# Kernel tuning notes

Measured on AMD Instinct MI355X. Metric: run time of the kernel, lower is better.

## Reference

```python
import jax, jax.numpy as jnp
import numpy as np

H = W = 32
K = 3


def _im2col(a):
    # a: [B, C, H, W] -> patches [B, H*W, C*K*K], channel-major (c, kh, kw)
    # matching torch.nn.Unfold ordering.
    a_pad = jnp.pad(a, ((0, 0), (0, 0), (1, 1), (1, 1)), mode='reflect')  # [B,C,H+2,W+2]
    cols = jnp.stack(
        [a_pad[:, :, kh:kh + H, kw:kw + W] for kh in range(K) for kw in range(K)],
        axis=2,
    )  # [B, C, 9, H, W]
    B, C = a.shape[0], a.shape[1]
    cols = cols.reshape(B, C * K * K, H * W)  # [B, 576, 1024]
    return jnp.swapaxes(cols, 1, 2)  # [B, 1024, 576]


def setup_inputs() -> dict:
    key = jax.random.key(0)
    k1, k2 = jax.random.split(key)
    a = jax.random.normal(k1, (256, 64, 32, 32), dtype=jnp.float32)
    # kaiming_uniform fan_in = 576 -> bound = sqrt(6/576)
    bound = float(np.sqrt(6.0 / 576.0))
    conv_kernel = jax.random.uniform(k2, (576, 64), dtype=jnp.float32,
                                     minval=-bound, maxval=bound)
    return {"a": a, "conv_kernel": conv_kernel}


def reference(a, conv_kernel):
    patches = _im2col(a)  # [B, 1024, 576]
    mean = jnp.mean(patches, axis=-1, keepdims=True)
    std = jnp.std(patches, axis=-1, keepdims=True, ddof=1)  # torch unbiased std
    normed = (patches - mean) / std
    out = jnp.einsum('blp,po->blo', normed, conv_kernel)  # [B, 1024, 64]
    # Fold with 1x1 kernel == reshape back to [B, 64, 32, 32]
    out = jnp.swapaxes(out, 1, 2).reshape(a.shape[0], conv_kernel.shape[1], H, W)
    return out
```

## Files before the change

kernel.cpp:

```cpp
#include <hip/hip_runtime.h>


#define STRIDE 68
#define NROW   10
#define NPIX   320

typedef __attribute__((ext_vector_type(8))) short bf16x8;
typedef __attribute__((ext_vector_type(4))) short bf16x4;
typedef __attribute__((ext_vector_type(4))) float f32x4;

__device__ __forceinline__ unsigned short f2bf(float f) {
    union { float f; unsigned u; } v; v.f = f;
    unsigned r = v.u + 0x7FFFu + ((v.u >> 16) & 1u);
    return (unsigned short)(r >> 16);
}

__device__ __forceinline__ int reflect32(int x) {
    x = (x < 0) ? -x : x;
    return (x > 31) ? (62 - x) : x;
}

__global__ void prep_kernel(const float* __restrict__ W, uint4* __restrict__ wf,
                            float* __restrict__ scolg) {
    if (blockIdx.x == 18) {
        __shared__ float red[256];
        int t = threadIdx.x;
        int o = t & 63, kq = t >> 6;
        float s = 0.f;
        for (int k = kq * 144; k < kq * 144 + 144; ++k) {
            union { unsigned u; float f; } cv;
            cv.u = ((unsigned)f2bf(W[k * 64 + o])) << 16;
            s += cv.f;
        }
        red[t] = s;
        __syncthreads();
        if (t < 64) scolg[t] = red[t] + red[t + 64] + red[t + 128] + red[t + 192];
        return;
    }
    int idx = blockIdx.x * 256 + threadIdx.x;
    int lane = idx & 63;
    int ks   = (idx >> 6) % 18;
    int ntg  = idx / 1152;
    int quad = lane >> 4;
    int o    = ntg * 16 + (lane & 15);
    unsigned short v[8];
    #pragma unroll
    for (int j = 0; j < 8; ++j) {
        int kp = ks * 32 + quad * 8 + j;
        int c  = kp & 63;
        int s  = kp >> 6;
        v[j] = f2bf(W[(c * 9 + s) * 64 + o]);
    }
    uint4 r;
    r.x = (unsigned)v[0] | ((unsigned)v[1] << 16);
    r.y = (unsigned)v[2] | ((unsigned)v[3] << 16);
    r.z = (unsigned)v[4] | ((unsigned)v[5] << 16);
    r.w = (unsigned)v[6] | ((unsigned)v[7] << 16);
    wf[idx] = r;
}

__global__ __launch_bounds__(512, 4)
void norm_conv_kernel(const float* __restrict__ a,
                      const uint4* __restrict__ wf,
                      const float* __restrict__ scolg,
                      float* __restrict__ out) {
    __shared__ unsigned short img[NPIX * STRIDE];
    __shared__ float sums[2 * NPIX];

    const int tid = threadIdx.x;
    const int b   = blockIdx.x >> 2;
    const int q   = blockIdx.x & 3;
    const int row_base = (q == 0) ? 0 : (q == 3 ? 22 : 8 * q - 1);
    const int lane = tid & 63;
    const int wid  = tid >> 6;
    const int quad = lane >> 4;
    const int mlan = lane & 15;

    const float* Ab = a + (size_t)b * 65536 + row_base * 32;
    for (int u = tid; u < 640; u += 512) {
        int p  = u >> 1;
        int ch = (u & 1) * 32;
        float s = 0.f, qq = 0.f;
        unsigned short* row = &img[p * STRIDE + ch];
        #pragma unroll
        for (int c4 = 0; c4 < 32; c4 += 4) {
            float v0 = Ab[(ch + c4) * 1024 + p];
            float v1 = Ab[(ch + c4 + 1) * 1024 + p];
            float v2 = Ab[(ch + c4 + 2) * 1024 + p];
            float v3 = Ab[(ch + c4 + 3) * 1024 + p];
            s  += (v0 + v1) + (v2 + v3);
            qq += (v0 * v0 + v1 * v1) + (v2 * v2 + v3 * v3);
            uint2 pk;
            pk.x = (unsigned)f2bf(v0) | ((unsigned)f2bf(v1) << 16);
            pk.y = (unsigned)f2bf(v2) | ((unsigned)f2bf(v3) << 16);
            *(uint2*)&row[c4] = pk;
        }
        s  += __shfl_xor(s, 1, 64);
        qq += __shfl_xor(qq, 1, 64);
        if ((u & 1) == 0) { sums[p] = s; sums[NPIX + p] = qq; }
    }
    __syncthreads();

    float mean = 0.f, inv = 0.f;
    if (tid < 256) {
        int hg = q * 8 + (tid >> 5);
        int wg = tid & 31;
        float s = 0.f, ss = 0.f;
        #pragma unroll
        for (int kh = 0; kh < 3; ++kh) {
            int hr = reflect32(hg + kh - 1) - row_base;
            #pragma unroll
            for (int kw = 0; kw < 3; ++kw) {
                int p = hr * 32 + reflect32(wg + kw - 1);
                s  += sums[p];
                ss += sums[NPIX + p];
            }
        }
        mean = s * (1.0f / 576.0f);
        inv  = rsqrtf((ss - s * mean) * (1.0f / 575.0f));
    }
    __syncthreads();
    if (tid < 256) { sums[tid * 2] = mean; sums[tid * 2 + 1] = inv; }
    __syncthreads();

    float So[4];
    #pragma unroll
    for (int nt = 0; nt < 4; ++nt) So[nt] = scolg[nt * 16 + mlan];

    int rowb[3], colb[2][3];
    #pragma unroll
    for (int kh = 0; kh < 3; ++kh)
        rowb[kh] = (reflect32(q * 8 + wid + kh - 1) - row_base) * (32 * STRIDE * 2) + quad * 16;
    #pragma unroll
    for (int j = 0; j < 2; ++j)
        #pragma unroll
        for (int kw = 0; kw < 3; ++kw)
            colb[j][kw] = reflect32(j * 16 + mlan + kw - 1) * (STRIDE * 2);

    f32x4 acc[2][4];
    #pragma unroll
    for (int mt = 0; mt < 2; ++mt)
        #pragma unroll
        for (int nt = 0; nt < 4; ++nt)
            acc[mt][nt] = (f32x4){0.f, 0.f, 0.f, 0.f};

    const uint4* bp = wf + lane;
    uint4 bnx[4];
    #pragma unroll
    for (int nt = 0; nt < 4; ++nt) bnx[nt] = bp[nt * 18 * 64];

    const char* imgc = (const char*)img;
    #pragma unroll
    for (int ks = 0; ks < 18; ++ks) {
        uint4 bc[4];
        #pragma unroll
        for (int nt = 0; nt < 4; ++nt) bc[nt] = bnx[nt];
        if (ks < 17) {
            #pragma unroll
            for (int nt = 0; nt < 4; ++nt) bnx[nt] = bp[(nt * 18 + ks + 1) * 64];
        }
        const int khi = (ks >> 1) / 3;
        const int kwi = (ks >> 1) % 3;
        const int coff = (ks & 1) * 64;
        #pragma unroll
        for (int mt = 0; mt < 2; ++mt) {
            int off = rowb[khi] + colb[mt][kwi] + coff;
            bf16x4 flo = *(const bf16x4*)(imgc + off);
            bf16x4 fhi = *(const bf16x4*)(imgc + off + 8);
            bf16x8 af  = __builtin_shufflevector(flo, fhi, 0, 1, 2, 3, 4, 5, 6, 7);
            #pragma unroll
            for (int nt = 0; nt < 4; ++nt) {
                union { uint4 u; bf16x8 v; } cb; cb.u = bc[nt];
                acc[mt][nt] = __builtin_amdgcn_mfma_f32_16x16x32_bf16(af, cb.v, acc[mt][nt], 0, 0, 0);
            }
        }
    }

    float* outB = out + (size_t)b * 65536 + q * 256;
    #pragma unroll
    for (int mt = 0; mt < 2; ++mt) {
        int l0 = (wid * 2 + mt) * 16 + quad * 4;
        float mn[4], iv[4];
        #pragma unroll
        for (int r = 0; r < 4; ++r) {
            mn[r] = sums[(l0 + r) * 2];
            iv[r] = sums[(l0 + r) * 2 + 1];
        }
        #pragma unroll
        for (int nt = 0; nt < 4; ++nt) {
            f32x4 rr;
            #pragma unroll
            for (int r = 0; r < 4; ++r)
                rr[r] = (acc[mt][nt][r] - mn[r] * So[nt]) * iv[r];
            *(f32x4*)(outB + (nt * 16 + mlan) * 1024 + l0) = rr;
        }
    }
}

extern "C" void kernel_launch(void* const* d_in, const int* in_sizes, int n_in,
                              void* d_out, int out_size, void* d_ws, size_t ws_size,
                              hipStream_t stream) {
    const float* a = (const float*)d_in[0];
    const float* w = (const float*)d_in[1];
    float* out = (float*)d_out;
    uint4* wf = (uint4*)d_ws;
    float* scolg = (float*)((char*)d_ws + 73728);
    prep_kernel<<<dim3(19), dim3(256), 0, stream>>>(w, wf, scolg);
    norm_conv_kernel<<<dim3(1024), dim3(512), 0, stream>>>(a, wf, scolg, out);
}
```

Before: 153.0 us.

## Warp-specialize conv kernel: producer waves double-buffer image quarters, consumers use 32x32 MFMA

Each block now processes a whole image, stepping through four row quarters. Four producer waves stage the next quarter into a double-buffered LDS tile while four consumer waves run the matmul. Consumers keep the full weight slice resident in registers and use 32x32x16 bf16 MFMA instead of 16x16x32. This removes redundant per-block weight reloads and overlaps global loads with compute. The cost is fewer blocks (256), much higher register and LDS use, and launch bounds lowered to 2 blocks per CU, which reduces occupancy and risks leaving CUs idle.

```diff
diff --git a/kernel.cpp b/kernel.cpp
--- a/kernel.cpp
+++ b/kernel.cpp
@@ -2,23 +2,28 @@
 
 
 #define STRIDE 68
-#define NROW   10
 #define NPIX   320
 
 typedef __attribute__((ext_vector_type(8))) short bf16x8;
 typedef __attribute__((ext_vector_type(4))) short bf16x4;
 typedef __attribute__((ext_vector_type(4))) float f32x4;
+typedef __attribute__((ext_vector_type(16))) float f32x16;
 
 __device__ __forceinline__ unsigned short f2bf(float f) {
     union { float f; unsigned u; } v; v.f = f;
     unsigned r = v.u + 0x7FFFu + ((v.u >> 16) & 1u);
     return (unsigned short)(r >> 16);
 }
-
+__device__ __forceinline__ float bf2f(unsigned short h) {
+    union { unsigned u; float f; } v; v.u = ((unsigned)h) << 16;
+    return v.f;
+}
 __device__ __forceinline__ int reflect32(int x) {
     x = (x < 0) ? -x : x;
     return (x > 31) ? (62 - x) : x;
 }
+
+__device__ __constant__ int c_rb[4] = {0, 7, 15, 22};
 
 __global__ void prep_kernel(const float* __restrict__ W, uint4* __restrict__ wf,
                             float* __restrict__ scolg) {
@@ -27,11 +32,8 @@
         int t = threadIdx.x;
         int o = t & 63, kq = t >> 6;
         float s = 0.f;
-        for (int k = kq * 144; k < kq * 144 + 144; ++k) {
-            union { unsigned u; float f; } cv;
-            cv.u = ((unsigned)f2bf(W[k * 64 + o])) << 16;
-            s += cv.f;
-        }
+        for (int k = kq * 144; k < kq * 144 + 144; ++k)
+            s += bf2f(f2bf(W[k * 64 + o]));
         red[t] = s;
         __syncthreads();
         if (t < 64) scolg[t] = red[t] + red[t + 64] + red[t + 128] + red[t + 192];
@@ -39,14 +41,14 @@
     }
     int idx = blockIdx.x * 256 + threadIdx.x;
     int lane = idx & 63;
-    int ks   = (idx >> 6) % 18;
-    int ntg  = idx / 1152;
-    int quad = lane >> 4;
-    int o    = ntg * 16 + (lane & 15);
+    int ks   = (idx >> 6) % 36;
+    int ntg  = idx / 2304;
+    int o    = ntg * 32 + (lane & 31);
+    int kb   = ks * 16 + (lane >> 5) * 8;
     unsigned short v[8];
     #pragma unroll
     for (int j = 0; j < 8; ++j) {
-        int kp = ks * 32 + quad * 8 + j;
+        int kp = kb + j;
         int c  = kp & 63;
         int s  = kp >> 6;
         v[j] = f2bf(W[(c * 9 + s) * 64 + o]);
@@ -59,140 +61,150 @@
     wf[idx] = r;
 }
 
-__global__ __launch_bounds__(512, 4)
+__device__ __forceinline__ void stage_quarter(const float* __restrict__ Ab, int ptid,
+                                              unsigned short* __restrict__ imgb,
+                                              float* __restrict__ sums4b) {
+    #pragma unroll
+    for (int k = 0; k < 5; ++k) {
+        int u  = k * 256 + ptid;
+        int cg = u / 320;
+        int p  = u - cg * 320;
+        float v[16];
+        #pragma unroll
+        for (int j = 0; j < 16; ++j)
+            v[j] = Ab[(cg * 16 + j) * 1024 + p];
+        float s = 0.f, ss = 0.f;
+        unsigned pk[8];
+        #pragma unroll
+        for (int j = 0; j < 8; ++j) {
+            float v0 = v[2 * j], v1 = v[2 * j + 1];
+            s  += v0 + v1;
+            ss += v0 * v0 + v1 * v1;
+            pk[j] = (unsigned)f2bf(v0) | ((unsigned)f2bf(v1) << 16);
+        }
+        unsigned short* row = &imgb[p * STRIDE + cg * 16];
+        #pragma unroll
+        for (int j = 0; j < 4; ++j) {
+            uint2 t; t.x = pk[2 * j]; t.y = pk[2 * j + 1];
+            *(uint2*)&row[j * 4] = t;
+        }
+        float2 sv; sv.x = s; sv.y = ss;
+        *(float2*)&sums4b[cg * (NPIX * 2) + p * 2] = sv;
+    }
+}
+
+__global__ __launch_bounds__(512, 2)
 void norm_conv_kernel(const float* __restrict__ a,
                       const uint4* __restrict__ wf,
                       const float* __restrict__ scolg,
                       float* __restrict__ out) {
-    __shared__ unsigned short img[NPIX * STRIDE];
-    __shared__ float sums[2 * NPIX];
-
-    const int tid = threadIdx.x;
-    const int b   = blockIdx.x >> 2;
-    const int q   = blockIdx.x & 3;
-    const int row_base = (q == 0) ? 0 : (q == 3 ? 22 : 8 * q - 1);
+    __shared__ unsigned short img[2][NPIX * STRIDE];
+    __shared__ float sums4[2][4 * NPIX * 2];
+    __shared__ float stats_s[4][256];
+
+    const int tid  = threadIdx.x;
     const int lane = tid & 63;
     const int wid  = tid >> 6;
-    const int quad = lane >> 4;
-    const int mlan = lane & 15;
-
-    const float* Ab = a + (size_t)b * 65536 + row_base * 32;
-    for (int u = tid; u < 640; u += 512) {
-        int p  = u >> 1;
-        int ch = (u & 1) * 32;
-        float s = 0.f, qq = 0.f;
-        unsigned short* row = &img[p * STRIDE + ch];
-        #pragma unroll
-        for (int c4 = 0; c4 < 32; c4 += 4) {
-            float v0 = Ab[(ch + c4) * 1024 + p];
-            float v1 = Ab[(ch + c4 + 1) * 1024 + p];
-            float v2 = Ab[(ch + c4 + 2) * 1024 + p];
-            float v3 = Ab[(ch + c4 + 3) * 1024 + p];
-            s  += (v0 + v1) + (v2 + v3);
-            qq += (v0 * v0 + v1 * v1) + (v2 * v2 + v3 * v3);
-            uint2 pk;
-            pk.x = (unsigned)f2bf(v0) | ((unsigned)f2bf(v1) << 16);
-            pk.y = (unsigned)f2bf(v2) | ((unsigned)f2bf(v3) << 16);
-            *(uint2*)&row[c4] = pk;
-        }
-        s  += __shfl_xor(s, 1, 64);
-        qq += __shfl_xor(qq, 1, 64);
-        if ((u & 1) == 0) { sums[p] = s; sums[NPIX + p] = qq; }
-    }
-    __syncthreads();
-
-    float mean = 0.f, inv = 0.f;
-    if (tid < 256) {
-        int hg = q * 8 + (tid >> 5);
-        int wg = tid & 31;
-        float s = 0.f, ss = 0.f;
-        #pragma unroll
-        for (int kh = 0; kh < 3; ++kh) {
-            int hr = reflect32(hg + kh - 1) - row_base;
+    const float* Aimg = a + (size_t)blockIdx.x * 65536;
+    float* outB = out + (size_t)blockIdx.x * 65536;
+
+    if (wid >= 4) {
+        const int ptid = tid - 256;
+        stage_quarter(Aimg + c_rb[0] * 32, ptid, img[0], sums4[0]);
+        __syncthreads();
+        for (int q = 0; q < 4; ++q) {
+            if (q < 3)
+                stage_quarter(Aimg + c_rb[q + 1] * 32, ptid,
+                              img[(q + 1) & 1], sums4[(q + 1) & 1]);
+            __syncthreads();
+        }
+    } else {
+        const int nt = wid & 1;
+        const int mq = wid >> 1;
+        const int nl = lane & 31;
+        const int hq = lane >> 5;
+
+        bf16x8 bfrag[36];
+        #pragma unroll
+        for (int ks = 0; ks < 36; ++ks) {
+            union { uint4 u; bf16x8 v; } cvt;
+            cvt.u = wf[(nt * 36 + ks) * 64 + lane];
+            bfrag[ks] = cvt.v;
+        }
+        const float So = scolg[nt * 32 + nl];
+        __syncthreads();
+
+        for (int q = 0; q < 4; ++q) {
+            const int cur = q & 1;
+            const int rb = c_rb[q];
+            const float* s4 = sums4[cur];
+
+            float st4[4];
             #pragma unroll
-            for (int kw = 0; kw < 3; ++kw) {
-                int p = hr * 32 + reflect32(wg + kw - 1);
-                s  += sums[p];
-                ss += sums[NPIX + p];
+            for (int e = 0; e < 2; ++e) {
+                int lq = mq * 128 + lane * 2 + e;
+                int hg = q * 8 + (lq >> 5);
+                int wg = lq & 31;
+                float s = 0.f, ss = 0.f;
+                #pragma unroll
+                for (int kh = 0; kh < 3; ++kh) {
+                    int hr = reflect32(hg + kh - 1) - rb;
+                    #pragma unroll
+                    for (int kw = 0; kw < 3; ++kw) {
+                        int p = hr * 32 + reflect32(wg + kw - 1);
+                        #pragma unroll
+                        for (int cg = 0; cg < 4; ++cg) {
+                            float2 sv = *(const float2*)&s4[cg * (NPIX * 2) + p * 2];
+                            s += sv.x; ss += sv.y;
+                        }
+                    }
+                }
+                float mean = s * (1.0f / 576.0f);
+                st4[e * 2]     = mean;
+                st4[e * 2 + 1] = rsqrtf((ss - s * mean) * (1.0f / 575.0f));
             }
-        }
-        mean = s * (1.0f / 576.0f);
-        inv  = rsqrtf((ss - s * mean) * (1.0f / 575.0f));
-    }
-    __syncthreads();
-    if (tid < 256) { sums[tid * 2] = mean; sums[tid * 2 + 1] = inv; }
-    __syncthreads();
-
-    float So[4];
-    #pragma unroll
-    for (int nt = 0; nt < 4; ++nt) So[nt] = scolg[nt * 16 + mlan];
-
-    int rowb[3], colb[2][3];
-    #pragma unroll
-    for (int kh = 0; kh < 3; ++kh)
-        rowb[kh] = (reflect32(q * 8 + wid + kh - 1) - row_base) * (32 * STRIDE * 2) + quad * 16;
-    #pragma unroll
-    for (int j = 0; j < 2; ++j)
-        #pragma unroll
-        for (int kw = 0; kw < 3; ++kw)
-            colb[j][kw] = reflect32(j * 16 + mlan + kw - 1) * (STRIDE * 2);
-
-    f32x4 acc[2][4];
-    #pragma unroll
-    for (int mt = 0; mt < 2; ++mt)
-        #pragma unroll
-        for (int nt = 0; nt < 4; ++nt)
-            acc[mt][nt] = (f32x4){0.f, 0.f, 0.f, 0.f};
-
-    const uint4* bp = wf + lane;
-    uint4 bnx[4];
-    #pragma unroll
-    for (int nt = 0; nt < 4; ++nt) bnx[nt] = bp[nt * 18 * 64];
-
-    const char* imgc = (const char*)img;
-    #pragma unroll
-    for (int ks = 0; ks < 18; ++ks) {
-        uint4 bc[4];
-        #pragma unroll
-        for (int nt = 0; nt < 4; ++nt) bc[nt] = bnx[nt];
-        if (ks < 17) {
-            #pragma unroll
-            for (int nt = 0; nt < 4; ++nt) bnx[nt] = bp[(nt * 18 + ks + 1) * 64];
-        }
-        const int khi = (ks >> 1) / 3;
-        const int kwi = (ks >> 1) % 3;
-        const int coff = (ks & 1) * 64;
-        #pragma unroll
-        for (int mt = 0; mt < 2; ++mt) {
-            int off = rowb[khi] + colb[mt][kwi] + coff;
-            bf16x4 flo = *(const bf16x4*)(imgc + off);
-            bf16x4 fhi = *(const bf16x4*)(imgc + off + 8);
-            bf16x8 af  = __builtin_shufflevector(flo, fhi, 0, 1, 2, 3, 4, 5, 6, 7);
-            #pragma unroll
-            for (int nt = 0; nt < 4; ++nt) {
-                union { uint4 u; bf16x8 v; } cb; cb.u = bc[nt];
-                acc[mt][nt] = __builtin_amdgcn_mfma_f32_16x16x32_bf16(af, cb.v, acc[mt][nt], 0, 0, 0);
+            f32x4 stw; stw[0] = st4[0]; stw[1] = st4[1]; stw[2] = st4[2]; stw[3] = st4[3];
+            *(f32x4*)&stats_s[wid][lane * 4] = stw;
+            __builtin_amdgcn_s_waitcnt(0);
+
+            const char* imgc = (const char*)img[cur];
+            for (int i = 0; i < 4; ++i) {
+                const int mt = mq * 4 + i;
+                const int hg = q * 8 + mt;
+                int base9[9];
+                #pragma unroll
+                for (int kh = 0; kh < 3; ++kh) {
+                    int hr = reflect32(hg + kh - 1) - rb;
+                    #pragma unroll
+                    for (int kw = 0; kw < 3; ++kw)
+                        base9[kh * 3 + kw] =
+                            ((hr * 32 + reflect32(nl + kw - 1)) * STRIDE + hq * 8) * 2;
+                }
+                f32x16 acc = {0.f,0.f,0.f,0.f,0.f,0.f,0.f,0.f,
+                              0.f,0.f,0.f,0.f,0.f,0.f,0.f,0.f};
+                #pragma unroll
+                for (int ks = 0; ks < 36; ++ks) {
+                    int off = base9[ks >> 2] + (ks & 3) * 32;
+                    bf16x4 flo = *(const bf16x4*)(imgc + off);
+                    bf16x4 fhi = *(const bf16x4*)(imgc + off + 8);
+                    bf16x8 af  = __builtin_shufflevector(flo, fhi, 0, 1, 2, 3, 4, 5, 6, 7);
+                    acc = __builtin_amdgcn_mfma_f32_32x32x16_bf16(af, bfrag[ks], acc, 0, 0, 0);
+                }
+                float* op = outB + (nt * 32 + nl) * 1024 + hg * 32;
+                #pragma unroll
+                for (int g = 0; g < 4; ++g) {
+                    int m0 = g * 8 + hq * 4;
+                    f32x4 st0 = *(const f32x4*)&stats_s[wid][(i * 32 + m0) * 2];
+                    f32x4 st1 = *(const f32x4*)&stats_s[wid][(i * 32 + m0) * 2 + 4];
+                    f32x4 rr;
+                    rr[0] = (acc[g * 4 + 0] - st0[0] * So) * st0[1];
+                    rr[1] = (acc[g * 4 + 1] - st0[2] * So) * st0[3];
+                    rr[2] = (acc[g * 4 + 2] - st1[0] * So) * st1[1];
+                    rr[3] = (acc[g * 4 + 3] - st1[2] * So) * st1[3];
+                    *(f32x4*)(op + m0) = rr;
+                }
             }
-        }
-    }
-
-    float* outB = out + (size_t)b * 65536 + q * 256;
-    #pragma unroll
-    for (int mt = 0; mt < 2; ++mt) {
-        int l0 = (wid * 2 + mt) * 16 + quad * 4;
-        float mn[4], iv[4];
-        #pragma unroll
-        for (int r = 0; r < 4; ++r) {
-            mn[r] = sums[(l0 + r) * 2];
-            iv[r] = sums[(l0 + r) * 2 + 1];
-        }
-        #pragma unroll
-        for (int nt = 0; nt < 4; ++nt) {
-            f32x4 rr;
-            #pragma unroll
-            for (int r = 0; r < 4; ++r)
-                rr[r] = (acc[mt][nt][r] - mn[r] * So[nt]) * iv[r];
-            *(f32x4*)(outB + (nt * 16 + mlan) * 1024 + l0) = rr;
+            __syncthreads();
         }
     }
 }
@@ -206,5 +218,5 @@
     uint4* wf = (uint4*)d_ws;
     float* scolg = (float*)((char*)d_ws + 73728);
     prep_kernel<<<dim3(19), dim3(256), 0, stream>>>(w, wf, scolg);
-    norm_conv_kernel<<<dim3(1024), dim3(512), 0, stream>>>(a, wf, scolg, out);
-}
+    norm_conv_kernel<<<dim3(256), dim3(512), 0, stream>>>(a, wf, scolg, out);
+}
```

Measured after the change: 142.5 us. -6.8%, faster.
